# Kernel tuning notes

Hardware: AMD Instinct MI355X
Metric: run time of the kernel (lower is better)

## Reference

```python
import jax, jax.numpy as jnp
import numpy as np

N_NODES = 16384
N_EDGES = 65536
N_GRAPHS = 512
F_XD = 78
HEADS = 10
HID = F_XD * HEADS  # 780
SEQ = 1000
EMB = 100
VOCAB = 8000
NF = 32
KS = 8
CLEN = EMB - KS + 1  # 93
OUT_DIM = 128


def setup_inputs():
    key = jax.random.key(0)
    keys = jax.random.split(key, 32)
    it = iter(keys)

    def rn(shape, scale=0.05):
        return jax.random.normal(next(it), shape, dtype=jnp.float32) * scale

    x = jax.random.normal(next(it), (N_NODES, F_XD), dtype=jnp.float32)
    edge_index = jax.random.randint(next(it), (2, N_EDGES), 0, N_NODES)
    batch = jnp.sort(jax.random.randint(next(it), (N_NODES,), 0, N_GRAPHS))
    target = jax.random.randint(next(it), (N_GRAPHS, SEQ), 0, VOCAB)
    return {
        "x": x, "edge_index": edge_index, "batch": batch, "target": target,
        "gat_w": rn((F_XD, HID)), "gat_att_src": rn((HEADS, F_XD)),
        "gat_att_dst": rn((HEADS, F_XD)), "gat_b": rn((HID,)),
        "gcn_w": rn((HID, HID)), "gcn_b": rn((HID,)),
        "fcg1_w": rn((2 * HID, 1500)), "fcg1_b": rn((1500,)),
        "fcg2_w": rn((1500, OUT_DIM)), "fcg2_b": rn((OUT_DIM,)),
        "emb_w": rn((VOCAB, EMB), 1.0),
        "conv_w": rn((NF, SEQ, KS)), "conv_b": rn((NF,)),
        "fcxt_w": rn((NF * CLEN, OUT_DIM)), "fcxt_b": rn((OUT_DIM,)),
        "mlp1_w": rn((2 * OUT_DIM, 1024)), "mlp1_b": rn((1024,)),
        "mlp2_w": rn((1024, 512)), "mlp2_b": rn((512,)),
        "mlp3_w": rn((512, 1)), "mlp3_b": rn((1,)),
    }


def _forward(edge_index, batch, target, x, gat_w, gat_att_src, gat_att_dst, gat_b,
             gcn_w, gcn_b, fcg1_w, fcg1_b, fcg2_w, fcg2_b, emb_w, conv_w, conv_b,
             fcxt_w, fcxt_b, mlp1_w, mlp1_b, mlp2_w, mlp2_b, mlp3_w, mlp3_b):
    loops = jnp.arange(N_NODES)
    src = jnp.concatenate([edge_index[0], loops])  # add self-loops (PyG default)
    dst = jnp.concatenate([edge_index[1], loops])
    # --- GATConv(78 -> 78, heads=10, concat) ---
    xh = (x @ gat_w).reshape(N_NODES, HEADS, F_XD)
    a_src = jnp.einsum('nhc,hc->nh', xh, gat_att_src)
    a_dst = jnp.einsum('nhc,hc->nh', xh, gat_att_dst)
    e = jax.nn.leaky_relu(a_src[src] + a_dst[dst], 0.2)  # [E+N, H]
    emax = jax.ops.segment_max(e, dst, num_segments=N_NODES)
    ee = jnp.exp(e - emax[dst])
    den = jax.ops.segment_sum(ee, dst, num_segments=N_NODES)
    coef = ee / den[dst]  # segment softmax over incoming edges
    h = jax.ops.segment_sum(xh[src] * coef[:, :, None], dst, num_segments=N_NODES)
    h = jax.nn.relu(h.reshape(N_NODES, HID) + gat_b)
    # --- GCNConv(780 -> 780), symmetric normalization with self-loops ---
    hw = h @ gcn_w
    deg = jax.ops.segment_sum(jnp.ones((src.shape[0],), hw.dtype), dst, num_segments=N_NODES)
    dinv = jax.lax.rsqrt(jnp.maximum(deg, 1.0))  # deg >= 1 due to self-loops
    g = jax.ops.segment_sum(hw[src] * (dinv[src] * dinv[dst])[:, None], dst,
                            num_segments=N_NODES) + gcn_b
    g = jax.nn.relu(g)
    # --- global max / mean pool per graph ---
    gmp = jax.ops.segment_max(g, batch, num_segments=N_GRAPHS)
    cnt = jax.ops.segment_sum(jnp.ones((N_NODES,), g.dtype), batch, num_segments=N_GRAPHS)
    gap = jax.ops.segment_sum(g, batch, num_segments=N_GRAPHS) / jnp.maximum(cnt, 1.0)[:, None]
    d = jnp.concatenate([gmp, gap], axis=1)  # [B, 1560]
    d = jax.nn.relu(d @ fcg1_w + fcg1_b)     # dropout = eval-mode no-op
    d = d @ fcg2_w + fcg2_b                  # [B, 128]
    # --- protein branch: embedding + Conv1d(in=1000, out=32, k=8) + fc ---
    emb = emb_w[target]  # [B, SEQ=1000, EMB=100]
    c = jax.lax.conv_general_dilated(emb, conv_w, (1,), 'VALID',
                                     dimension_numbers=('NCH', 'OIH', 'NCH'))
    c = c + conv_b[None, :, None]            # [B, 32, 93]
    p = c.reshape(N_GRAPHS, NF * CLEN) @ fcxt_w + fcxt_b  # [B, 128]
    # --- fused MLP head: 256 -> 1024 -> 512 -> 1 ---
    o = jnp.concatenate([d, p], axis=1)
    o = jax.nn.relu(o @ mlp1_w + mlp1_b)
    o = jax.nn.relu(o @ mlp2_w + mlp2_b)
    return o @ mlp3_w + mlp3_b               # [B, 1]


def reference(x, edge_index, batch, target, gat_w, gat_att_src, gat_att_dst, gat_b,
              gcn_w, gcn_b, fcg1_w, fcg1_b, fcg2_w, fcg2_b, emb_w, conv_w, conv_b,
              fcxt_w, fcxt_b, mlp1_w, mlp1_b, mlp2_w, mlp2_b, mlp3_w, mlp3_b):
    return _forward(edge_index, batch, target, x, gat_w, gat_att_src, gat_att_dst,
                    gat_b, gcn_w, gcn_b, fcg1_w, fcg1_b, fcg2_w, fcg2_b, emb_w,
                    conv_w, conv_b, fcxt_w, fcxt_b, mlp1_w, mlp1_b, mlp2_w, mlp2_b,
                    mlp3_w, mlp3_b)
```

## Files before the change

kernel.cpp:

```cpp
#include <hip/hip_runtime.h>

#define NN 16384
#define NE 65536
#define NT 81920
#define NG 512
#define NH 10
#define FX 78
#define HD 780
#define SEQ 1000
#define EMB 100
#define NF 32
#define KS 8
#define CLEN 93

typedef __bf16 bf16x8 __attribute__((ext_vector_type(8)));
typedef float  f32x4  __attribute__((ext_vector_type(4)));

__device__ inline void load_lds16(const void* g, void* l)
{
    __builtin_amdgcn_global_load_lds(
        (const __attribute__((address_space(1))) void*)g,
        (__attribute__((address_space(3))) void*)l, 16, 0, 0);
}

__global__ __launch_bounds__(256)
void preproc_all(const float* __restrict__ emb_w, __bf16* __restrict__ embbf,
                 const float* __restrict__ conv_w, __bf16* __restrict__ w2,
                 const float* __restrict__ x, __bf16* __restrict__ Abf,
                 const int* __restrict__ batch, int* __restrict__ goffs)
{
    long idx = (long)blockIdx.x*256 + threadIdx.x;
    if (idx < 896112L) {
        int r = idx / 112, c = idx - (long)(idx/112)*112;
        embbf[idx] = (__bf16)((r < 8000 && c < EMB) ? emb_w[(size_t)r*EMB + c] : 0.f);
        return;
    }
    idx -= 896112L;
    if (idx < 262144L) {
        int op = idx >> 10, i = idx & 1023;
        int o = op & 31, k = op >> 5;
        w2[idx] = (i < SEQ) ? (__bf16)conv_w[((size_t)o*SEQ + i)*KS + k] : (__bf16)0.f;
        return;
    }
    idx -= 262144L;
    if (idx < 1572864L) {
        int r = idx / 96, c = idx - (long)(idx/96)*96;
        Abf[idx] = (c < FX) ? (__bf16)x[(size_t)r*FX + c] : (__bf16)0.f;
        return;
    }
    idx -= 1572864L;
    if (idx <= NG) {
        int b = (int)idx;
        if (b == NG) { goffs[NG] = NN; return; }
        int lo = 0, hi = NN;
        while (lo < hi) { int mid = (lo+hi) >> 1; if (batch[mid] < b) lo = mid+1; else hi = mid; }
        goffs[b] = lo;
    }
}
#define PRE_TOTAL 2731633L
#define PRE_BLOCKS ((PRE_TOTAL + 255) / 256)

__global__ __launch_bounds__(256)
void transpose_w(const float* __restrict__ fcg1_w, __bf16* __restrict__ wg1,
                 const float* __restrict__ gcn_w,  __bf16* __restrict__ wgcn,
                 const float* __restrict__ gat_w,  __bf16* __restrict__ wgat,
                 const float* __restrict__ fcg2_w, __bf16* __restrict__ wg2,
                 const float* __restrict__ fcxt_w, __bf16* __restrict__ wxt,
                 const float* __restrict__ mlp1_w, __bf16* __restrict__ wm1,
                 const float* __restrict__ mlp2_w, __bf16* __restrict__ wm2)
{
    __shared__ float tile[32][33];
    int t = blockIdx.x;
    const float* B; __bf16* out; int K, N, Kp, tk_n;
    if (t < 2352)              { B=fcg1_w; out=wg1;  K=1560; N=1500; Kp=1568; tk_n=49; }
    else if ((t -= 2352) < 700){ B=gcn_w;  out=wgcn; K=780;  N=780;  Kp=800;  tk_n=25; }
    else if ((t -= 700) < 84)  { B=gat_w;  out=wgat; K=78;   N=780;  Kp=96;   tk_n=3;  }
    else if ((t -= 84) < 188)  { B=fcg2_w; out=wg2;  K=1500; N=128;  Kp=1504; tk_n=47; }
    else if ((t -= 188) < 372) { B=fcxt_w; out=wxt;  K=2976; N=128;  Kp=2976; tk_n=93; }
    else if ((t -= 372) < 256) { B=mlp1_w; out=wm1;  K=256;  N=1024; Kp=256;  tk_n=8;  }
    else { t -= 256;             B=mlp2_w; out=wm2;  K=1024; N=512;  Kp=1024; tk_n=32; }
    int k0 = (t % tk_n) * 32, n0 = (t / tk_n) * 32;
    int jj = threadIdx.x & 31, ii0 = threadIdx.x >> 5;
#pragma unroll
    for (int g = 0; g < 4; g++) {
        int i = ii0 + g*8;
        int gk = k0 + i, gn = n0 + jj;
        tile[i][jj] = (gk < K && gn < N) ? B[(size_t)gk*N + gn] : 0.f;
    }
    __syncthreads();
#pragma unroll
    for (int g = 0; g < 4; g++) {
        int i = ii0 + g*8;
        out[(size_t)(n0 + i)*Kp + k0 + jj] = (__bf16)tile[jj][i];
    }
}
#define TRANS_BLOCKS 4464

template<bool BIAS, bool RELU, bool BF16OUT>
__global__ __launch_bounds__(512)
void gemm_mfma(const __bf16* __restrict__ A, const __bf16* __restrict__ Bt,
               const float* __restrict__ bias, void* __restrict__ Cv,
               int M, int N, int Kp, int ldc, int Nz)
{
    __shared__ __align__(16) __bf16 As[128*32];
    __shared__ __align__(16) __bf16 Bs[128*32];
    const int tid = threadIdx.x;
    const int nbx = gridDim.x;
    const int lin = blockIdx.y * nbx + blockIdx.x;
    const int per = (nbx * gridDim.y) >> 3;
    const int logical = (lin & 7) * per + (lin >> 3);
    const int row0 = (logical / nbx) * 128, col0 = (logical % nbx) * 128;
    const int lane = tid & 63, wid = tid >> 6;
    const int wm = wid & 3, wn = wid >> 2;
    const int l15 = lane & 15, lk = lane >> 4;
    const int sr  = tid >> 2;
    const int sc8 = (tid & 3) * 8;

    f32x4 acc[2][4];
#pragma unroll
    for (int i = 0; i < 2; i++)
#pragma unroll
        for (int j = 0; j < 4; j++) acc[i][j] = (f32x4){0.f,0.f,0.f,0.f};

    for (int k0 = 0; k0 < Kp; k0 += 32) {
        __syncthreads();
        load_lds16(A  + (size_t)(row0+sr)*Kp + k0 + sc8, &As[wid*512]);
        load_lds16(Bt + (size_t)(col0+sr)*Kp + k0 + sc8, &Bs[wid*512]);
        __syncthreads();
        bf16x8 af[2], bfr[4];
#pragma unroll
        for (int i = 0; i < 2; i++)
            af[i]  = *(const bf16x8*)&As[(wm*32 + i*16 + l15)*32 + lk*8];
#pragma unroll
        for (int j = 0; j < 4; j++)
            bfr[j] = *(const bf16x8*)&Bs[(wn*64 + j*16 + l15)*32 + lk*8];
#pragma unroll
        for (int i = 0; i < 2; i++)
#pragma unroll
            for (int j = 0; j < 4; j++)
                acc[i][j] = __builtin_amdgcn_mfma_f32_16x16x32_bf16(af[i], bfr[j], acc[i][j], 0, 0, 0);
    }

#pragma unroll
    for (int i = 0; i < 2; i++) {
        int rbase = row0 + wm*32 + i*16 + lk*4;
#pragma unroll
        for (int j = 0; j < 4; j++) {
            int cc = col0 + wn*64 + j*16 + l15;
            if (cc >= Nz) continue;
            bool real = cc < N;
            float bv = (BIAS && real) ? bias[cc] : 0.f;
#pragma unroll
            for (int r = 0; r < 4; r++) {
                float v = real ? (acc[i][j][r] + bv) : 0.f;
                if (RELU) v = v > 0.f ? v : 0.f;
                if (BF16OUT) ((__bf16*)Cv)[(size_t)(rbase + r)*ldc + cc] = (__bf16)v;
                else         ((float*) Cv)[(size_t)(rbase + r)*ldc + cc] = v;
            }
        }
    }
}

#define BKP 40
__global__ __launch_bounds__(256)
void gemm_mfma_splitk(const __bf16* __restrict__ A, const __bf16* __restrict__ Bt,
                      float* __restrict__ part, int M, int Kp, int ldp, int ksteps)
{
    __shared__ __align__(16) __bf16 As[128*BKP];
    __shared__ __align__(16) __bf16 Bs[128*BKP];
    const int tid = threadIdx.x;
    const int row0 = blockIdx.y*128, col0 = blockIdx.x*128;
    const int s = blockIdx.z;
    const int lane = tid & 63, wid = tid >> 6;
    const int wm = wid & 1, wn = wid >> 1;
    const int l15 = lane & 15, lk = lane >> 4;

    const int T = Kp >> 5;
    int kb = s*ksteps, ke = kb + ksteps;
    if (ke > T) ke = T;

    f32x4 acc[4][4];
#pragma unroll
    for (int i = 0; i < 4; i++)
#pragma unroll
        for (int j = 0; j < 4; j++) acc[i][j] = (f32x4){0.f,0.f,0.f,0.f};

    for (int kk = kb; kk < ke; kk++) {
        int k0 = kk*32;
        __syncthreads();
#pragma unroll
        for (int it = 0; it < 2; ++it) {
            int c = tid + it*256;
            int r = c >> 2, c16 = c & 3;
            uint4 va = *(const uint4*)(A  + (size_t)(row0+r)*Kp + k0 + c16*8);
            *(uint4*)&As[r*BKP + c16*8] = va;
            uint4 vb = *(const uint4*)(Bt + (size_t)(col0+r)*Kp + k0 + c16*8);
            *(uint4*)&Bs[r*BKP + c16*8] = vb;
        }
        __syncthreads();
        bf16x8 af[4], bfr[4];
#pragma unroll
        for (int i = 0; i < 4; i++) {
            af[i]  = *(const bf16x8*)&As[(wm*64 + i*16 + l15)*BKP + lk*8];
            bfr[i] = *(const bf16x8*)&Bs[(wn*64 + i*16 + l15)*BKP + lk*8];
        }
#pragma unroll
        for (int i = 0; i < 4; i++)
#pragma unroll
            for (int j = 0; j < 4; j++)
                acc[i][j] = __builtin_amdgcn_mfma_f32_16x16x32_bf16(af[i], bfr[j], acc[i][j], 0, 0, 0);
    }

#pragma unroll
    for (int i = 0; i < 4; i++) {
        int rbase = row0 + wm*64 + i*16 + lk*4;
#pragma unroll
        for (int j = 0; j < 4; j++) {
            int cc = col0 + wn*64 + j*16 + l15;
#pragma unroll
            for (int r = 0; r < 4; r++)
                part[((size_t)s*M + rbase + r)*ldp + cc] = acc[i][j][r];
        }
    }
}

template<bool RELU>
__global__ __launch_bounds__(256)
void reduce_splitk(const float* __restrict__ part, const float* __restrict__ bias,
                   __bf16* __restrict__ C, int M, int N, int ldp, int S,
                   int ldc, int Nz)
{
    int idx = blockIdx.x*256 + threadIdx.x;
    int nc4 = Nz >> 2;
    if (idx >= M*nc4) return;
    int r = idx / nc4, c = (idx - r*nc4)*4;
    float4 a = {0.f,0.f,0.f,0.f};
    for (int s = 0; s < S; s++) {
        float4 v = *(const float4*)(part + ((size_t)s*M + r)*ldp + c);
        a.x += v.x; a.y += v.y; a.z += v.z; a.w += v.w;
    }
    float vv[4] = {a.x, a.y, a.z, a.w};
    __bf16 o4[4];
#pragma unroll
    for (int j = 0; j < 4; j++) {
        float v = 0.f;
        if (c + j < N) {
            v = vv[j] + bias[c+j];
            if (RELU) v = v > 0.f ? v : 0.f;
        }
        o4[j] = (__bf16)v;
    }
    *(uint2*)&C[(size_t)r*ldc + c] = *(uint2*)o4;
}

__global__ __launch_bounds__(256)
void attn_logits(const __bf16* __restrict__ xh, const float* __restrict__ att_s,
                 const float* __restrict__ att_d,
                 float* __restrict__ a_src, float* __restrict__ a_dst)
{
    int idx = blockIdx.x*256 + threadIdx.x;
    if (idx >= NN*NH) return;
    int n = idx / NH, h = idx % NH;
    const __bf16* xr = xh + (size_t)n*800 + h*FX;
    const float* as = att_s + h*FX;
    const float* ad = att_d + h*FX;
    float s1 = 0.f, s2 = 0.f;
    for (int c = 0; c < FX; c++) {
        float v = (float)xr[c];
        s1 = fmaf(v, as[c], s1);
        s2 = fmaf(v, ad[c], s2);
    }
    a_src[idx] = s1;
    a_dst[idx] = s2;
}

__global__ void edge_count(const int* __restrict__ ei, int* __restrict__ deg)
{
    int e = blockIdx.x*256 + threadIdx.x;
    if (e >= NT) return;
    int dst = (e < NE) ? ei[NE + e] : (e - NE);
    atomicAdd(&deg[dst], 1);
}

__global__ __launch_bounds__(1024)
void scan_kernel(const int* __restrict__ deg, int* __restrict__ offs,
                 int* __restrict__ cursor, float* __restrict__ dinv)
{
    __shared__ int part[1024];
    int tid = threadIdx.x;
    int base = tid*16;
    int v[16]; int ssum = 0;
#pragma unroll
    for (int j = 0; j < 16; j++) {
        v[j] = deg[base+j];
        dinv[base+j] = rsqrtf((float)(v[j] > 0 ? v[j] : 1));
        ssum += v[j];
    }
    part[tid] = ssum;
    __syncthreads();
    for (int d = 1; d < 1024; d <<= 1) {
        int t = (tid >= d) ? part[tid-d] : 0;
        __syncthreads();
        part[tid] += t;
        __syncthreads();
    }
    int run = (tid == 0) ? 0 : part[tid-1];
#pragma unroll
    for (int j = 0; j < 16; j++) { offs[base+j] = run; cursor[base+j] = run; run += v[j]; }
    if (tid == 1023) offs[NN] = run;
}

__global__ void edge_scatter(const int* __restrict__ ei, int* __restrict__ cursor,
                             int* __restrict__ csr)
{
    int e = blockIdx.x*256 + threadIdx.x;
    if (e >= NT) return;
    int src, dst;
    if (e < NE) { src = ei[e]; dst = ei[NE + e]; }
    else        { src = e - NE; dst = e - NE; }
    int pos = atomicAdd(&cursor[dst], 1);
    csr[pos] = src;
}

__global__ __launch_bounds__(256)
void gat_agg(const __bf16* __restrict__ xh, const float* __restrict__ a_src,
             const float* __restrict__ a_dst, const float* __restrict__ gat_b,
             const int* __restrict__ offs, const int* __restrict__ csr,
             __bf16* __restrict__ hbf)
{
    int n = blockIdx.x*4 + (threadIdx.x >> 6);
    if (n >= NN) return;
    int lane = threadIdx.x & 63;
    bool act = lane < 60;
    int h   = act ? (lane / 6) : 0;
    int sub = act ? (lane % 6) : 0;
    int cbase = h*FX + sub*13;
    int off = offs[n], end = offs[n+1];
    float adn = a_dst[n*NH + h];

    float m = -3.0e38f;
    for (int i = off; i < end; i++) {
        int s = csr[i];
        float ev = a_src[s*NH + h] + adn;
        ev = ev > 0.f ? ev : 0.2f*ev;
        m = fmaxf(m, ev);
    }
    float den = 0.f;
    float acc[13];
#pragma unroll
    for (int j = 0; j < 13; j++) acc[j] = 0.f;
    for (int i = off; i < end; i++) {
        int s = csr[i];
        float ev = a_src[s*NH + h] + adn;
        ev = ev > 0.f ? ev : 0.2f*ev;
        float ee = __expf(ev - m);
        den += ee;
        const __bf16* xr = xh + (size_t)s*800 + cbase;
#pragma unroll
        for (int j = 0; j < 13; j++) acc[j] = fmaf((float)xr[j], ee, acc[j]);
    }
    if (act) {
        float inv = 1.f / den;
        const float* bb = gat_b + cbase;
        __bf16* op = hbf + (size_t)n*800 + cbase;
#pragma unroll
        for (int j = 0; j < 13; j++) {
            float v = fmaf(acc[j], inv, bb[j]);
            op[j] = (__bf16)(v > 0.f ? v : 0.f);
        }
    } else {
        __bf16* op = hbf + (size_t)n*800 + 780 + (lane - 60)*5;
#pragma unroll
        for (int j = 0; j < 5; j++) op[j] = (__bf16)0.f;
    }
}

__global__ __launch_bounds__(256)
void gcn_agg(const __bf16* __restrict__ hw, const float* __restrict__ dinv,
             const float* __restrict__ gcn_b, const int* __restrict__ offs,
             const int* __restrict__ csr, __bf16* __restrict__ g)
{
    int n = blockIdx.x*4 + (threadIdx.x >> 6);
    if (n >= NN) return;
    int lane = threadIdx.x & 63;
    int off = offs[n], end = offs[n+1];
    float dn = dinv[n];
    float acc[13];
#pragma unroll
    for (int j = 0; j < 13; j++) acc[j] = 0.f;
    for (int i = off; i < end; i++) {
        int s = csr[i];
        float w = dinv[s] * dn;
        const __bf16* r = hw + (size_t)s*800;
#pragma unroll
        for (int j = 0; j < 13; j++) {
            int c = lane + 64*j;
            if (c < HD) acc[j] = fmaf((float)r[c], w, acc[j]);
        }
    }
    __bf16* op = g + (size_t)n*HD;
#pragma unroll
    for (int j = 0; j < 13; j++) {
        int c = lane + 64*j;
        if (c < HD) {
            float v = acc[j] + gcn_b[c];
            op[c] = (__bf16)(v > 0.f ? v : 0.f);
        }
    }
}

__global__ __launch_bounds__(256)
void pool_kernel(const __bf16* __restrict__ g, const int* __restrict__ goffs,
                 __bf16* __restrict__ d)
{
    int b = blockIdx.x;
    int tid = threadIdx.x;
    int s = goffs[b], e = goffs[b+1];
    float mx[4], sm[4];
#pragma unroll
    for (int j = 0; j < 4; j++) { mx[j] = -3.0e38f; sm[j] = 0.f; }
    for (int n = s; n < e; n++) {
        const __bf16* r = g + (size_t)n*HD;
#pragma unroll
        for (int j = 0; j < 4; j++) {
            int c = tid + 256*j;
            if (c < HD) { float v = (float)r[c]; mx[j] = fmaxf(mx[j], v); sm[j] += v; }
        }
    }
    int cnt = e - s;
    float inv = 1.f / (float)(cnt > 0 ? cnt : 1);
#pragma unroll
    for (int j = 0; j < 4; j++) {
        int c = tid + 256*j;
        if (c < HD) {
            d[(size_t)b*1568 + c]      = (__bf16)mx[j];
            d[(size_t)b*1568 + HD + c] = (__bf16)(sm[j] * inv);
        }
    }
    if (tid < 8) d[(size_t)b*1568 + 1560 + tid] = (__bf16)0.f;
}

#define CP 104
#define SB (112*40)

__global__ __launch_bounds__(512)
void conv_gemm2(const int* __restrict__ target, const __bf16* __restrict__ embbf,
                const __bf16* __restrict__ w2, const float* __restrict__ conv_b,
                __bf16* __restrict__ cbuf)
{
    __shared__ __align__(16) __bf16 Pl[256*CP];
    __bf16* Bs = Pl;
    int* tg = (int*)&Pl[2*SB];
    const int b = blockIdx.x;
    const int tid = threadIdx.x;
    const int w = tid >> 6, lane = tid & 63;
    const int l15 = lane & 15, lk = lane >> 4;

    for (int i = tid; i < 1024; i += 512)
        tg[i] = ((i < SEQ) ? target[b*SEQ + i] : 8000) * 112;
    __syncthreads();

    const bool st = tid < 448;
    const int sr  = tid & 31;
    const int sch = tid >> 5;

    uint4 sv;
    auto stage_load = [&](int p) {
        if (!st) return;
        sv = *(const uint4*)((const ushort*)embbf + tg[p*32 + sr] + sch*8);
    };
    auto stage_write = [&](int buf) {
        if (!st) return;
        const __bf16* s8 = (const __bf16*)&sv;
        __bf16* base = &Bs[buf*SB + (sch*8)*40 + sr];
#pragma unroll
        for (int j = 0; j < 8; j++) base[j*40] = s8[j];
    };

    f32x4 acc[7][2];
#pragma unroll
    for (int i = 0; i < 7; i++) {
        acc[i][0] = (f32x4){0.f,0.f,0.f,0.f};
        acc[i][1] = (f32x4){0.f,0.f,0.f,0.f};
    }

    const __bf16* w2w0 = w2 + (size_t)(w*32 + l15)*1024 + lk*8;
    const __bf16* w2w1 = w2w0 + (size_t)16*1024;

    stage_load(0);
    stage_write(0);
    int cur = 0;
    for (int p = 0; p < 32; ++p) {
        __syncthreads();
        if (p+1 < 32) stage_load(p+1);
        bf16x8 bf0 = *(const bf16x8*)(w2w0 + p*32);
        bf16x8 bf1 = *(const bf16x8*)(w2w1 + p*32);
        const __bf16* bsc = Bs + cur*SB + lk*8;
        __builtin_amdgcn_s_setprio(1);
#pragma unroll
        for (int mt = 0; mt < 7; mt++) {
            bf16x8 af = *(const bf16x8*)(bsc + (mt*16 + l15)*40);
            acc[mt][0] = __builtin_amdgcn_mfma_f32_16x16x32_bf16(af, bf0, acc[mt][0], 0, 0, 0);
            acc[mt][1] = __builtin_amdgcn_mfma_f32_16x16x32_bf16(af, bf1, acc[mt][1], 0, 0, 0);
        }
        __builtin_amdgcn_s_setprio(0);
        if (p+1 < 32) stage_write(cur^1);
        cur ^= 1;
    }

    __syncthreads();
#pragma unroll
    for (int mt = 0; mt < 7; mt++) {
#pragma unroll
        for (int nt = 0; nt < 2; nt++) {
            int op = w*32 + nt*16 + l15;
            int c0 = mt*16 + lk*4;
            if (c0 >= 100) continue;
            __bf16 o4[4];
#pragma unroll
            for (int rr = 0; rr < 4; rr++) o4[rr] = (__bf16)acc[mt][nt][rr];
            *(uint2*)&Pl[op*CP + c0] = *(uint2*)o4;
        }
    }
    __syncthreads();

    {
        int o = tid & 31, tg16 = tid >> 5;
        float cb = conv_b[o];
#pragma unroll
        for (int j = 0; j < 6; j++) {
            int t = tg16*6 + j;
            if (t >= CLEN) continue;
            float s = cb;
#pragma unroll
            for (int k = 0; k < 8; k++)
                s += (float)Pl[(k*32 + o)*CP + t + k];
            cbuf[(size_t)b*2976 + o*CLEN + t] = (__bf16)s;
        }
    }
}

__global__ __launch_bounds__(256)
void mlp3_dot(const __bf16* __restrict__ o2, const float* __restrict__ w,
              const float* __restrict__ bias, float* __restrict__ out)
{
    int row = blockIdx.x*4 + (threadIdx.x >> 6);
    int lane = threadIdx.x & 63;
    bf16x8 v = *(const bf16x8*)(o2 + (size_t)row*512 + lane*8);
    float4 w0 = *(const float4*)(w + lane*8);
    float4 w1 = *(const float4*)(w + lane*8 + 4);
    float s = (float)v[0]*w0.x + (float)v[1]*w0.y + (float)v[2]*w0.z + (float)v[3]*w0.w
            + (float)v[4]*w1.x + (float)v[5]*w1.y + (float)v[6]*w1.z + (float)v[7]*w1.w;
#pragma unroll
    for (int off = 32; off > 0; off >>= 1) s += __shfl_down(s, off);
    if (lane == 0) out[row] = s + bias[0];
}

extern "C" void kernel_launch(void* const* d_in, const int* in_sizes, int n_in,
                              void* d_out, int out_size, void* d_ws, size_t ws_size,
                              hipStream_t stream)
{
    const float* x      = (const float*)d_in[0];
    const int*   ei     = (const int*)  d_in[1];
    const int*   batch  = (const int*)  d_in[2];
    const int*   target = (const int*)  d_in[3];
    const float* gat_w  = (const float*)d_in[4];
    const float* att_s  = (const float*)d_in[5];
    const float* att_d  = (const float*)d_in[6];
    const float* gat_b  = (const float*)d_in[7];
    const float* gcn_w  = (const float*)d_in[8];
    const float* gcn_b  = (const float*)d_in[9];
    const float* fcg1_w = (const float*)d_in[10];
    const float* fcg1_b = (const float*)d_in[11];
    const float* fcg2_w = (const float*)d_in[12];
    const float* fcg2_b = (const float*)d_in[13];
    const float* emb_w  = (const float*)d_in[14];
    const float* conv_w = (const float*)d_in[15];
    const float* conv_b = (const float*)d_in[16];
    const float* fcxt_w = (const float*)d_in[17];
    const float* fcxt_b = (const float*)d_in[18];
    const float* mlp1_w = (const float*)d_in[19];
    const float* mlp1_b = (const float*)d_in[20];
    const float* mlp2_w = (const float*)d_in[21];
    const float* mlp2_b = (const float*)d_in[22];
    const float* mlp3_w = (const float*)d_in[23];
    const float* mlp3_b = (const float*)d_in[24];
    float* out = (float*)d_out;

    char* ws = (char*)d_ws;
    size_t off = 0;
    auto alloc = [&](size_t bytes) -> char* {
        char* p = ws + off;
        off = (off + bytes + 255) & ~(size_t)255;
        return p;
    };
    __bf16* xhbf  = (__bf16*)alloc((size_t)NN*800*2);
    __bf16* g     = (__bf16*)alloc((size_t)NN*HD*2);
    char*  hbf_rg = alloc((size_t)NN*800*2);
    __bf16* Abf   = (__bf16*)hbf_rg;
    __bf16* hbf   = (__bf16*)hbf_rg;
    float* partial= (float*)hbf_rg;
    __bf16* wgat  = (__bf16*)alloc((size_t)896*96*2);
    __bf16* wgcn  = (__bf16*)alloc((size_t)896*800*2);
    __bf16* wg1   = (__bf16*)alloc((size_t)1536*1568*2);
    __bf16* wg2   = (__bf16*)alloc((size_t)128*1504*2);
    __bf16* wxt   = (__bf16*)alloc((size_t)128*2976*2);
    __bf16* wm1   = (__bf16*)alloc((size_t)1024*256*2);
    __bf16* wm2   = (__bf16*)alloc((size_t)512*1024*2);
    __bf16* convw2= (__bf16*)alloc((size_t)256*1024*2);
    __bf16* embbf = (__bf16*)alloc((size_t)8001*112*2);
    float* a_src  = (float*)alloc((size_t)NN*NH*4);
    float* a_dst  = (float*)alloc((size_t)NN*NH*4);
    int*   deg    = (int*)alloc((size_t)NN*4);
    int*   offs   = (int*)alloc((size_t)(NN+1)*4);
    int*   cursor = (int*)alloc((size_t)NN*4);
    int*   csr    = (int*)alloc((size_t)NT*4);
    float* dinv   = (float*)alloc((size_t)NN*4);
    int*   goffs  = (int*)alloc((size_t)(NG+1)*4);
    __bf16* dpool = (__bf16*)alloc((size_t)NG*1568*2);
    __bf16* d1bf  = (__bf16*)alloc((size_t)NG*1504*2);
    __bf16* cbuf  = (__bf16*)alloc((size_t)NG*NF*CLEN*2);
    __bf16* obuf  = (__bf16*)alloc((size_t)NG*256*2);
    __bf16* o1bf  = (__bf16*)alloc((size_t)NG*1024*2);
    __bf16* o2bf  = (__bf16*)alloc((size_t)NG*512*2);

    __bf16* hwbf = xhbf;

    hipMemsetAsync(deg, 0, (size_t)NN*4, stream);

    preproc_all<<<dim3((unsigned)PRE_BLOCKS), 256, 0, stream>>>(
        emb_w, embbf, conv_w, convw2, x, Abf, batch, goffs);
    transpose_w<<<dim3(TRANS_BLOCKS), 256, 0, stream>>>(
        fcg1_w, wg1, gcn_w, wgcn, gat_w, wgat, fcg2_w, wg2,
        fcxt_w, wxt, mlp1_w, wm1, mlp2_w, wm2);

    conv_gemm2<<<dim3(NG), 512, 0, stream>>>(target, embbf, convw2, conv_b, cbuf);

    gemm_mfma<false,false,true>
        <<<dim3(7, NN/128), 512, 0, stream>>>(Abf, wgat, nullptr, xhbf, NN, HD, 96, 800, 800);
    attn_logits<<<dim3((NN*NH+255)/256), 256, 0, stream>>>(xhbf, att_s, att_d, a_src, a_dst);

    edge_count  <<<dim3(NT/256), 256, 0, stream>>>(ei, deg);
    scan_kernel <<<1, 1024, 0, stream>>>(deg, offs, cursor, dinv);
    edge_scatter<<<dim3(NT/256), 256, 0, stream>>>(ei, cursor, csr);

    gat_agg<<<dim3(NN/4), 256, 0, stream>>>(xhbf, a_src, a_dst, gat_b, offs, csr, hbf);

    gemm_mfma<false,false,true>
        <<<dim3(7, NN/128), 512, 0, stream>>>(hbf, wgcn, nullptr, hwbf, NN, HD, 800, 800, 800);
    gcn_agg<<<dim3(NN/4), 256, 0, stream>>>(hwbf, dinv, gcn_b, offs, csr, g);

    pool_kernel<<<NG, 256, 0, stream>>>(g, goffs, dpool);

    gemm_mfma_splitk<<<dim3(12, 4, 4), 256, 0, stream>>>(dpool, wg1, partial, NG, 1568, 1536, 13);
    reduce_splitk<true><<<dim3((NG*(1504/4)+255)/256), 256, 0, stream>>>(partial, fcg1_b, d1bf, NG, 1500, 1536, 4, 1504, 1504);
    gemm_mfma_splitk<<<dim3(1, 4, 12), 256, 0, stream>>>(d1bf, wg2, partial, NG, 1504, 128, 4);
    reduce_splitk<false><<<dim3((NG*32+255)/256), 256, 0, stream>>>(partial, fcg2_b, obuf, NG, 128, 128, 12, 256, 128);
    gemm_mfma_splitk<<<dim3(1, 4, 24), 256, 0, stream>>>(cbuf, wxt, partial, NG, 2976, 128, 4);
    reduce_splitk<false><<<dim3((NG*32+255)/256), 256, 0, stream>>>(partial, fcxt_b, obuf + 128, NG, 128, 128, 24, 256, 128);
    gemm_mfma_splitk<<<dim3(8, 4, 2), 256, 0, stream>>>(obuf, wm1, partial, NG, 256, 1024, 4);
    reduce_splitk<true><<<dim3((NG*256+255)/256), 256, 0, stream>>>(partial, mlp1_b, o1bf, NG, 1024, 1024, 2, 1024, 1024);
    gemm_mfma_splitk<<<dim3(4, 4, 8), 256, 0, stream>>>(o1bf, wm2, partial, NG, 1024, 512, 4);
    reduce_splitk<true><<<dim3((NG*128+255)/256), 256, 0, stream>>>(partial, mlp2_b, o2bf, NG, 512, 512, 8, 512, 512);

    mlp3_dot<<<dim3(NG/4), 256, 0, stream>>>(o2bf, mlp3_w, mlp3_b, out);
}
```

Measured before the change: 352.7 us.

## Split conv GEMM over sequence halves with LDS atomic tap reduction

The protein Conv1d GEMM is split along the 1000-long sequence dimension into two grid slices. This doubles the block count from 512 to 1024 and halves each block's serial K loop. Each block folds the 8 kernel taps into a shared float buffer with LDS atomics instead of staging bf16 results and summing them afterwards. A new reduce kernel adds the two partials plus bias into the bf16 output, which costs an extra launch and an fp32 partial buffer round-trip.

Measured after the change: 479.5 us. 1.36x slower.

```diff
diff --git a/kernel.cpp b/kernel.cpp
--- a/kernel.cpp
+++ b/kernel.cpp
@@ -440,24 +440,25 @@
     if (tid < 8) d[(size_t)b*1568 + 1560 + tid] = (__bf16)0.f;
 }
 
-#define CP 104
-#define SB (112*40)
+#define SBc (112*40)
 
 __global__ __launch_bounds__(512)
-void conv_gemm2(const int* __restrict__ target, const __bf16* __restrict__ embbf,
-                const __bf16* __restrict__ w2, const float* __restrict__ conv_b,
-                __bf16* __restrict__ cbuf)
-{
-    __shared__ __align__(16) __bf16 Pl[256*CP];
-    __bf16* Bs = Pl;
-    int* tg = (int*)&Pl[2*SB];
-    const int b = blockIdx.x;
+void conv_gemm3(const int* __restrict__ target, const __bf16* __restrict__ embbf,
+                const __bf16* __restrict__ w2, float* __restrict__ cpart)
+{
+    __shared__ __align__(16) __bf16 Bs[2*SBc];
+    __shared__ int tg[512];
+    __shared__ float cl[32*97];
+    const int b = blockIdx.x, z = blockIdx.y;
     const int tid = threadIdx.x;
     const int w = tid >> 6, lane = tid & 63;
     const int l15 = lane & 15, lk = lane >> 4;
 
-    for (int i = tid; i < 1024; i += 512)
-        tg[i] = ((i < SEQ) ? target[b*SEQ + i] : 8000) * 112;
+    {
+        int k = z*512 + tid;
+        tg[tid] = ((k < SEQ) ? target[b*SEQ + k] : 8000) * 112;
+    }
+    for (int i = tid; i < 32*97; i += 512) cl[i] = 0.f;
     __syncthreads();
 
     const bool st = tid < 448;
@@ -472,7 +473,7 @@
     auto stage_write = [&](int buf) {
         if (!st) return;
         const __bf16* s8 = (const __bf16*)&sv;
-        __bf16* base = &Bs[buf*SB + (sch*8)*40 + sr];
+        __bf16* base = &Bs[buf*SBc + (sch*8)*40 + sr];
 #pragma unroll
         for (int j = 0; j < 8; j++) base[j*40] = s8[j];
     };
@@ -484,18 +485,18 @@
         acc[i][1] = (f32x4){0.f,0.f,0.f,0.f};
     }
 
-    const __bf16* w2w0 = w2 + (size_t)(w*32 + l15)*1024 + lk*8;
+    const __bf16* w2w0 = w2 + (size_t)(w*32 + l15)*1024 + z*512 + lk*8;
     const __bf16* w2w1 = w2w0 + (size_t)16*1024;
 
     stage_load(0);
     stage_write(0);
     int cur = 0;
-    for (int p = 0; p < 32; ++p) {
+    for (int p = 0; p < 16; ++p) {
         __syncthreads();
-        if (p+1 < 32) stage_load(p+1);
+        if (p+1 < 16) stage_load(p+1);
         bf16x8 bf0 = *(const bf16x8*)(w2w0 + p*32);
         bf16x8 bf1 = *(const bf16x8*)(w2w1 + p*32);
-        const __bf16* bsc = Bs + cur*SB + lk*8;
+        const __bf16* bsc = Bs + cur*SBc + lk*8;
         __builtin_amdgcn_s_setprio(1);
 #pragma unroll
         for (int mt = 0; mt < 7; mt++) {
@@ -504,7 +505,7 @@
             acc[mt][1] = __builtin_amdgcn_mfma_f32_16x16x32_bf16(af, bf1, acc[mt][1], 0, 0, 0);
         }
         __builtin_amdgcn_s_setprio(0);
-        if (p+1 < 32) stage_write(cur^1);
+        if (p+1 < 16) stage_write(cur^1);
         cur ^= 1;
     }
 
@@ -513,31 +514,38 @@
     for (int mt = 0; mt < 7; mt++) {
 #pragma unroll
         for (int nt = 0; nt < 2; nt++) {
-            int op = w*32 + nt*16 + l15;
-            int c0 = mt*16 + lk*4;
-            if (c0 >= 100) continue;
-            __bf16 o4[4];
-#pragma unroll
-            for (int rr = 0; rr < 4; rr++) o4[rr] = (__bf16)acc[mt][nt][rr];
-            *(uint2*)&Pl[op*CP + c0] = *(uint2*)o4;
+            int o = nt*16 + l15;
+#pragma unroll
+            for (int rr = 0; rr < 4; rr++) {
+                int t = mt*16 + lk*4 + rr - w;
+                if (t >= 0 && t < CLEN)
+                    atomicAdd(&cl[o*97 + t], acc[mt][nt][rr]);
+            }
         }
     }
     __syncthreads();
-
     {
-        int o = tid & 31, tg16 = tid >> 5;
-        float cb = conv_b[o];
+        int o = tid & 31, grp = tid >> 5;
+        float* dst = cpart + ((size_t)(z*NG + b))*3072 + o*96;
 #pragma unroll
         for (int j = 0; j < 6; j++) {
-            int t = tg16*6 + j;
-            if (t >= CLEN) continue;
-            float s = cb;
-#pragma unroll
-            for (int k = 0; k < 8; k++)
-                s += (float)Pl[(k*32 + o)*CP + t + k];
-            cbuf[(size_t)b*2976 + o*CLEN + t] = (__bf16)s;
-        }
-    }
+            int t = grp*6 + j;
+            dst[t] = (t < CLEN) ? cl[o*97 + t] : 0.f;
+        }
+    }
+}
+
+__global__ __launch_bounds__(256)
+void conv_reduce(const float* __restrict__ cpart, const float* __restrict__ conv_b,
+                 __bf16* __restrict__ cbuf)
+{
+    int idx = blockIdx.x*256 + threadIdx.x;
+    if (idx >= NG*NF*CLEN) return;
+    int b = idx / 2976, rem = idx - b*2976;
+    int o = rem / 93, t = rem - o*93;
+    size_t src = (size_t)b*3072 + o*96 + t;
+    float v = cpart[src] + cpart[(size_t)NG*3072 + src] + conv_b[o];
+    cbuf[idx] = (__bf16)v;
 }
 
 __global__ __launch_bounds__(256)
@@ -609,6 +617,7 @@
     __bf16* wm2   = (__bf16*)alloc((size_t)512*1024*2);
     __bf16* convw2= (__bf16*)alloc((size_t)256*1024*2);
     __bf16* embbf = (__bf16*)alloc((size_t)8001*112*2);
+    float* cpart  = (float*)alloc((size_t)2*NG*3072*4);
     float* a_src  = (float*)alloc((size_t)NN*NH*4);
     float* a_dst  = (float*)alloc((size_t)NN*NH*4);
     int*   deg    = (int*)alloc((size_t)NN*4);
@@ -634,7 +643,8 @@
         fcg1_w, wg1, gcn_w, wgcn, gat_w, wgat, fcg2_w, wg2,
         fcxt_w, wxt, mlp1_w, wm1, mlp2_w, wm2);
 
-    conv_gemm2<<<dim3(NG), 512, 0, stream>>>(target, embbf, convw2, conv_b, cbuf);
+    conv_gemm3<<<dim3(NG, 2), 512, 0, stream>>>(target, embbf, convw2, cpart);
+    conv_reduce<<<dim3((NG*NF*CLEN + 255)/256), 256, 0, stream>>>(cpart, conv_b, cbuf);
 
     gemm_mfma<false,false,true>
         <<<dim3(7, NN/128), 512, 0, stream>>>(Abf, wgat, nullptr, xhbf, NN, HD, 96, 800, 800);
```
